# Kernel tuning notes

Measured on AMD Instinct MI355X. Metric: run time of the kernel, lower is better.

Reference implementation:

```python
import jax, jax.numpy as jnp
import numpy as np

N, INC, INN, OUTC, OUTN, MAXD = 8, 64, 20000, 64, 8000, 32


def setup_inputs() -> dict:
    key = jax.random.key(0)
    k0, k1, k2, k3, k4 = jax.random.split(key, 5)
    # adjacency list: outn nodes, degree in [8, 32], padded to MAXD with index 0
    rng = np.random.default_rng(0)
    deg = rng.integers(8, MAXD + 1, size=OUTN)                      # (outn,)
    A_np = rng.integers(0, INN, size=(OUTN, MAXD))                  # (outn, maxD)
    valid = np.arange(MAXD)[None, :] < deg[:, None]
    A_np = np.where(valid, A_np, 0)
    # '_norm' option: mask entries are 1/degree for valid slots, 0 for pad
    mask_np = valid.astype(np.float32) / deg[:, None].astype(np.float32)

    x = jax.random.normal(k0, (N, INC, INN), dtype=jnp.float32)
    # hadamard weight: sqrt(2/inn) * U(-1, 1)
    weight = np.sqrt(2.0 / INN).astype(np.float32) * (
        2.0 * jax.random.uniform(k1, (INC, INN), dtype=jnp.float32) - 1.0)
    # weight_norm Linear(inc, outc): v (outc, inc) direction, g (outc,) magnitude
    ct_v = jax.random.normal(k2, (OUTC, INC), dtype=jnp.float32) * (1.0 / np.sqrt(INC).astype(np.float32))
    ct_g = 0.5 + jax.random.uniform(k3, (OUTC,), dtype=jnp.float32)
    bias = 0.2 * jax.random.normal(k4, (1, OUTC, OUTN), dtype=jnp.float32)
    return {
        'x': x,
        'weight': weight,
        'ct_v': ct_v,
        'ct_g': ct_g,
        'bias': bias,
        'mask': jnp.asarray(mask_np),
        'A': jnp.asarray(A_np, dtype=jnp.int32),
    }


def reference(x, weight, ct_v, ct_g, bias, mask, A):
    # x: (N, inc, inn); weight: (inc, inn)
    xw = x * weight                                   # hadamard
    gathered = xw[:, :, A]                            # (N, inc, outn, maxD) adjacency gather
    pooled = jnp.einsum('bcod,od->bco', gathered, mask)  # degree-normalized masked sum
    # weight_norm: W = g * v / ||v||_row
    W = ct_g[:, None] * ct_v / jnp.linalg.norm(ct_v, axis=1, keepdims=True)  # (outc, inc)
    y = jnp.einsum('bco,kc->bko', pooled, W)          # (N, outc, outn)
    return y + bias
```

## Files before the change

kernel.cpp:

```cpp
#include <hip/hip_runtime.h>
#include <stdint.h>

#define NB   8
#define INC  64
#define INN  20000
#define OUTC 64
#define OUTN 8000
#define MAXD 32

__device__ __forceinline__ uint32_t pack_bf16_2(float a, float b) {
    uint32_t ua = __float_as_uint(a);
    uint32_t ub = __float_as_uint(b);
    uint32_t ra = (ua + 0x7FFFu + ((ua >> 16) & 1u)) >> 16;
    uint32_t rb = (ub + 0x7FFFu + ((ub >> 16) & 1u)) >> 16;
    return (ra & 0xFFFFu) | (rb << 16);
}

__global__ void prep_kernel(const int* __restrict__ A, const float* __restrict__ mask,
                            const float* __restrict__ ct_v, const float* __restrict__ ct_g,
                            uint4* __restrict__ AQ, float2* __restrict__ scale2,
                            float* __restrict__ W_T) {
    if (blockIdx.x == 64) {
        int k = threadIdx.x;
        if (k < OUTC) {
            float s = 0.f;
            for (int c = 0; c < INC; ++c) { float v = ct_v[k * INC + c]; s += v * v; }
            float inv = ct_g[k] / sqrtf(s);
            for (int c = 0; c < INC; ++c) W_T[c * OUTC + k] = ct_v[k * INC + c] * inv;
        }
        return;
    }
    int o = blockIdx.x * 128 + threadIdx.x;
    if (o >= OUTN) return;
    const int4* arow = (const int4*)(A + (size_t)o * MAXD);
#pragma unroll
    for (int j = 0; j < 4; ++j) {
        int4 v0 = arow[2 * j];
        int4 v1 = arow[2 * j + 1];
        uint4 pk;
        pk.x = (uint32_t)v0.x | ((uint32_t)v0.y << 16);
        pk.y = (uint32_t)v0.z | ((uint32_t)v0.w << 16);
        pk.z = (uint32_t)v1.x | ((uint32_t)v1.y << 16);
        pk.w = (uint32_t)v1.z | ((uint32_t)v1.w << 16);
        AQ[(size_t)j * OUTN + o] = pk;
    }
    float invdeg = mask[(size_t)o * MAXD];
    float deg    = rintf(1.0f / invdeg);
    scale2[o] = make_float2(invdeg, 32.0f - deg);
}

__global__ __launch_bounds__(1024, 8)
void gather_kernel(const float* __restrict__ x, const float* __restrict__ w,
                   const uint4* __restrict__ AQ, const float2* __restrict__ scale2,
                   float* __restrict__ pooled) {
    __shared__ __align__(16) uint32_t smem[INN];
    int h = blockIdx.x;
    int g = blockIdx.y;
    int b = blockIdx.z;
    int tid = threadIdx.x;
    int c0 = g * 2;

    const float* xb = x + ((size_t)b * INC + c0) * INN;
    const float* wb = w + (size_t)c0 * INN;
    for (int p = tid; p < INN / 4; p += 1024) {
        int i = p * 4;
        float4 x0 = *(const float4*)(xb + i);
        float4 x1 = *(const float4*)(xb + INN + i);
        float4 w0 = *(const float4*)(wb + i);
        float4 w1 = *(const float4*)(wb + INN + i);
        uint4 pk;
        pk.x = pack_bf16_2(x0.x * w0.x, x1.x * w1.x);
        pk.y = pack_bf16_2(x0.y * w0.y, x1.y * w1.y);
        pk.z = pack_bf16_2(x0.z * w0.z, x1.z * w1.z);
        pk.w = pack_bf16_2(x0.w * w0.w, x1.w * w1.w);
        *(uint4*)&smem[i] = pk;
    }
    __syncthreads();

    uint32_t z = smem[0];
    float z0 = __uint_as_float(z << 16);
    float z1 = __uint_as_float(z & 0xFFFF0000u);

    const char* sbase = (const char*)smem;
    int obase = h * (OUTN / 2);
    int oend  = obase + (OUTN / 2);
#pragma unroll
    for (int it = 0; it < 4; ++it) {
        int o = obase + tid + it * 1024;
        if (o < oend) {
            uint32_t q[16];
#pragma unroll
            for (int j = 0; j < 4; ++j) {
                uint4 v = AQ[(size_t)j * OUTN + o];
                q[j * 4 + 0] = v.x; q[j * 4 + 1] = v.y;
                q[j * 4 + 2] = v.z; q[j * 4 + 3] = v.w;
            }
            float a0 = 0.f, a1 = 0.f;
#pragma unroll
            for (int p = 0; p < 16; ++p) {
                uint32_t u   = q[p];
                int off0 = (int)(u & 0xFFFFu) << 2;
                int off1 = (int)(u >> 16) << 2;
                uint32_t v0 = *(const uint32_t*)(sbase + off0);
                uint32_t v1 = *(const uint32_t*)(sbase + off1);
                a0 += __uint_as_float(v0 << 16);
                a1 += __uint_as_float(v0 & 0xFFFF0000u);
                a0 += __uint_as_float(v1 << 16);
                a1 += __uint_as_float(v1 & 0xFFFF0000u);
            }
            float2 sc = scale2[o];
            a0 = (a0 - sc.y * z0) * sc.x;
            a1 = (a1 - sc.y * z1) * sc.x;
            pooled[((size_t)(b * OUTC + c0 + 0)) * OUTN + o] = a0;
            pooled[((size_t)(b * OUTC + c0 + 1)) * OUTN + o] = a1;
        }
    }
}

__global__ __launch_bounds__(256)
void out_kernel(float* io, const float* __restrict__ W_T,
                const float* __restrict__ bias) {
    __shared__ __align__(16) float sp[INC][128];
    __shared__ __align__(16) float sw[INC][OUTC];
    int obase = blockIdx.x * 128;
    int b     = blockIdx.y;

    const float* pb = io + (size_t)b * INC * OUTN;
    for (int idx = threadIdx.x; idx < INC * 32; idx += 256) {
        int c  = idx >> 5;
        int q  = idx & 31;
        int o4 = obase + q * 4;
        float4 v = (o4 < OUTN) ? *(const float4*)(pb + (size_t)c * OUTN + o4)
                               : make_float4(0.f, 0.f, 0.f, 0.f);
        *(float4*)(&sp[c][q * 4]) = v;
    }
    for (int idx = threadIdx.x; idx < (INC * OUTC) / 4; idx += 256) {
        ((float4*)sw)[idx] = ((const float4*)W_T)[idx];
    }
    __syncthreads();

    int t   = threadIdx.x;
    int kt  = t >> 4;
    int ot0 = (t & 15) * 8;
    int k0  = kt * 4;

    float acc[4][8];
#pragma unroll
    for (int kk = 0; kk < 4; ++kk) {
#pragma unroll
        for (int jh = 0; jh < 2; ++jh) {
            int o4 = obase + ot0 + jh * 4;
            float4 bv = (o4 < OUTN)
                ? *(const float4*)(bias + (size_t)(k0 + kk) * OUTN + o4)
                : make_float4(0.f, 0.f, 0.f, 0.f);
            acc[kk][jh * 4 + 0] = bv.x;
            acc[kk][jh * 4 + 1] = bv.y;
            acc[kk][jh * 4 + 2] = bv.z;
            acc[kk][jh * 4 + 3] = bv.w;
        }
    }

#pragma unroll 4
    for (int c = 0; c < INC; ++c) {
        float4 w4  = *(const float4*)(&sw[c][k0]);
        float4 pa  = *(const float4*)(&sp[c][ot0]);
        float4 pb4 = *(const float4*)(&sp[c][ot0 + 4]);
        float p[8] = {pa.x, pa.y, pa.z, pa.w, pb4.x, pb4.y, pb4.z, pb4.w};
        float wv[4] = {w4.x, w4.y, w4.z, w4.w};
#pragma unroll
        for (int kk = 0; kk < 4; ++kk)
#pragma unroll
            for (int j = 0; j < 8; ++j)
                acc[kk][j] += wv[kk] * p[j];
    }

    int o0 = obase + ot0;
    if (o0 < OUTN) {
#pragma unroll
        for (int kk = 0; kk < 4; ++kk) {
            float4 s0 = make_float4(acc[kk][0], acc[kk][1], acc[kk][2], acc[kk][3]);
            float4 s1 = make_float4(acc[kk][4], acc[kk][5], acc[kk][6], acc[kk][7]);
            float* dst = io + ((size_t)(b * OUTC + k0 + kk)) * OUTN + o0;
            *(float4*)(dst)     = s0;
            *(float4*)(dst + 4) = s1;
        }
    }
}

extern "C" void kernel_launch(void* const* d_in, const int* in_sizes, int n_in,
                              void* d_out, int out_size, void* d_ws, size_t ws_size,
                              hipStream_t stream) {
    const float* x    = (const float*)d_in[0];
    const float* w    = (const float*)d_in[1];
    const float* ct_v = (const float*)d_in[2];
    const float* ct_g = (const float*)d_in[3];
    const float* bias = (const float*)d_in[4];
    const float* mask = (const float*)d_in[5];
    const int*   A    = (const int*)d_in[6];
    float* y = (float*)d_out;

    char* ws = (char*)d_ws;
    uint4*  AQ     = (uint4*)(ws);
    float2* scale2 = (float2*)(ws + 512000);
    float*  W_T    = (float*)(ws + 576000);

    prep_kernel<<<65, 128, 0, stream>>>(A, mask, ct_v, ct_g, AQ, scale2, W_T);
    gather_kernel<<<dim3(2, 32, NB), 1024, 0, stream>>>(x, w, AQ, scale2, y);
    out_kernel<<<dim3(63, NB), 256, 0, stream>>>(y, W_T, bias);
}
```

Baseline: 52.38 us.

## Transpose hadamard product to node-major bf16 and gather rows from global/L2

The prep kernel now computes x*w in bf16 and writes it transposed as (batch, node, channel), so each input node's 64 channels sit in one 128-byte row. The gather kernel assigns one wavefront per output node, with lanes mapping to channels. Neighbour indices are broadcast with readfirstlane, and each neighbour becomes one coalesced row read from global/L2 instead of an LDS gather. Results are transposed through shared memory for coalesced stores. This replaces the per-block 80 KB LDS staging, in which x was reread 2x across halves. The cost is an extra 20 MB workspace round trip and random row accesses that rely on L2/MALL hits.

```diff
diff --git a/kernel.cpp b/kernel.cpp
--- a/kernel.cpp
+++ b/kernel.cpp
@@ -8,111 +8,149 @@
 #define OUTN 8000
 #define MAXD 32
 
-__device__ __forceinline__ uint32_t pack_bf16_2(float a, float b) {
-    uint32_t ua = __float_as_uint(a);
-    uint32_t ub = __float_as_uint(b);
-    uint32_t ra = (ua + 0x7FFFu + ((ua >> 16) & 1u)) >> 16;
-    uint32_t rb = (ub + 0x7FFFu + ((ub >> 16) & 1u)) >> 16;
-    return (ra & 0xFFFFu) | (rb << 16);
-}
-
-__global__ void prep_kernel(const int* __restrict__ A, const float* __restrict__ mask,
-                            const float* __restrict__ ct_v, const float* __restrict__ ct_g,
-                            uint4* __restrict__ AQ, float2* __restrict__ scale2,
-                            float* __restrict__ W_T) {
-    if (blockIdx.x == 64) {
-        int k = threadIdx.x;
-        if (k < OUTC) {
-            float s = 0.f;
-            for (int c = 0; c < INC; ++c) { float v = ct_v[k * INC + c]; s += v * v; }
-            float inv = ct_g[k] / sqrtf(s);
-            for (int c = 0; c < INC; ++c) W_T[c * OUTC + k] = ct_v[k * INC + c] * inv;
-        }
+__global__ __launch_bounds__(256)
+void xt_prep_kernel(const float* __restrict__ x, const float* __restrict__ w,
+                    const int* __restrict__ A, const float* __restrict__ mask,
+                    const float* __restrict__ ct_v, const float* __restrict__ ct_g,
+                    ushort* __restrict__ xT, uint4* __restrict__ AQ,
+                    float2* __restrict__ scale2, float* __restrict__ W_T) {
+    int t = threadIdx.x;
+    if (blockIdx.y == 8) {
+        int flat = blockIdx.x;
+        if (flat == 64) {
+            int k = t;
+            if (k < OUTC) {
+                float s = 0.f;
+                for (int c = 0; c < INC; ++c) { float v = ct_v[k * INC + c]; s += v * v; }
+                float inv = ct_g[k] / sqrtf(s);
+                for (int c = 0; c < INC; ++c) W_T[c * OUTC + k] = ct_v[k * INC + c] * inv;
+            }
+            return;
+        }
+        if (flat > 64 || t >= 128) return;
+        int o = flat * 128 + t;
+        if (o >= OUTN) return;
+        const int4* arow = (const int4*)(A + (size_t)o * MAXD);
+#pragma unroll
+        for (int j = 0; j < 4; ++j) {
+            int4 v0 = arow[2 * j];
+            int4 v1 = arow[2 * j + 1];
+            uint4 pk;
+            pk.x = (uint32_t)(v0.x << 1) | ((uint32_t)(v0.y << 1) << 16);
+            pk.y = (uint32_t)(v0.z << 1) | ((uint32_t)(v0.w << 1) << 16);
+            pk.z = (uint32_t)(v1.x << 1) | ((uint32_t)(v1.y << 1) << 16);
+            pk.w = (uint32_t)(v1.z << 1) | ((uint32_t)(v1.w << 1) << 16);
+            AQ[(size_t)j * OUTN + o] = pk;
+        }
+        float invdeg = mask[(size_t)o * MAXD];
+        float deg    = rintf(1.0f / invdeg);
+        scale2[o] = make_float2(invdeg, 32.0f - deg);
         return;
     }
-    int o = blockIdx.x * 128 + threadIdx.x;
-    if (o >= OUTN) return;
-    const int4* arow = (const int4*)(A + (size_t)o * MAXD);
-#pragma unroll
-    for (int j = 0; j < 4; ++j) {
-        int4 v0 = arow[2 * j];
-        int4 v1 = arow[2 * j + 1];
-        uint4 pk;
-        pk.x = (uint32_t)v0.x | ((uint32_t)v0.y << 16);
-        pk.y = (uint32_t)v0.z | ((uint32_t)v0.w << 16);
-        pk.z = (uint32_t)v1.x | ((uint32_t)v1.y << 16);
-        pk.w = (uint32_t)v1.z | ((uint32_t)v1.w << 16);
-        AQ[(size_t)j * OUTN + o] = pk;
-    }
-    float invdeg = mask[(size_t)o * MAXD];
-    float deg    = rintf(1.0f / invdeg);
-    scale2[o] = make_float2(invdeg, 32.0f - deg);
-}
-
-__global__ __launch_bounds__(1024, 8)
-void gather_kernel(const float* __restrict__ x, const float* __restrict__ w,
-                   const uint4* __restrict__ AQ, const float2* __restrict__ scale2,
-                   float* __restrict__ pooled) {
-    __shared__ __align__(16) uint32_t smem[INN];
-    int h = blockIdx.x;
-    int g = blockIdx.y;
-    int b = blockIdx.z;
-    int tid = threadIdx.x;
-    int c0 = g * 2;
-
-    const float* xb = x + ((size_t)b * INC + c0) * INN;
-    const float* wb = w + (size_t)c0 * INN;
-    for (int p = tid; p < INN / 4; p += 1024) {
-        int i = p * 4;
-        float4 x0 = *(const float4*)(xb + i);
-        float4 x1 = *(const float4*)(xb + INN + i);
-        float4 w0 = *(const float4*)(wb + i);
-        float4 w1 = *(const float4*)(wb + INN + i);
-        uint4 pk;
-        pk.x = pack_bf16_2(x0.x * w0.x, x1.x * w1.x);
-        pk.y = pack_bf16_2(x0.y * w0.y, x1.y * w1.y);
-        pk.z = pack_bf16_2(x0.z * w0.z, x1.z * w1.z);
-        pk.w = pack_bf16_2(x0.w * w0.w, x1.w * w1.w);
-        *(uint4*)&smem[i] = pk;
+
+    __shared__ ushort tile[64][68];
+    int b  = blockIdx.y;
+    int i0 = blockIdx.x * 64;
+    int il = (t & 15) * 4;
+    int cb = t >> 4;
+
+#pragma unroll
+    for (int cl = 0; cl < 4; ++cl) {
+        int c = cb + cl * 16;
+        int i = i0 + il;
+        if (i < INN) {
+            float4 xv = *(const float4*)(x + ((size_t)b * INC + c) * INN + i);
+            float4 wv = *(const float4*)(w + (size_t)c * INN + i);
+            float p0 = xv.x * wv.x, p1 = xv.y * wv.y, p2 = xv.z * wv.z, p3 = xv.w * wv.w;
+            uint32_t u0 = (__float_as_uint(p0) + 0x7FFFu + ((__float_as_uint(p0) >> 16) & 1u)) >> 16;
+            uint32_t u1 = (__float_as_uint(p1) + 0x7FFFu + ((__float_as_uint(p1) >> 16) & 1u)) >> 16;
+            uint32_t u2 = (__float_as_uint(p2) + 0x7FFFu + ((__float_as_uint(p2) >> 16) & 1u)) >> 16;
+            uint32_t u3 = (__float_as_uint(p3) + 0x7FFFu + ((__float_as_uint(p3) >> 16) & 1u)) >> 16;
+            uint2 pk = make_uint2((u0 & 0xFFFFu) | (u1 << 16), (u2 & 0xFFFFu) | (u3 << 16));
+            *(uint2*)(&tile[c][il]) = pk;
+        }
     }
     __syncthreads();
 
-    uint32_t z = smem[0];
-    float z0 = __uint_as_float(z << 16);
-    float z1 = __uint_as_float(z & 0xFFFF0000u);
-
-    const char* sbase = (const char*)smem;
-    int obase = h * (OUTN / 2);
-    int oend  = obase + (OUTN / 2);
-#pragma unroll
-    for (int it = 0; it < 4; ++it) {
-        int o = obase + tid + it * 1024;
-        if (o < oend) {
-            uint32_t q[16];
-#pragma unroll
-            for (int j = 0; j < 4; ++j) {
-                uint4 v = AQ[(size_t)j * OUTN + o];
-                q[j * 4 + 0] = v.x; q[j * 4 + 1] = v.y;
-                q[j * 4 + 2] = v.z; q[j * 4 + 3] = v.w;
+    int i_loc = t >> 2;
+    int h     = t & 3;
+    int i     = i0 + i_loc;
+    if (i < INN) {
+        ushort s[16];
+#pragma unroll
+        for (int j = 0; j < 16; ++j) s[j] = tile[h * 16 + j][i_loc];
+        uint4 a0, a1;
+        a0.x = (uint32_t)s[0]  | ((uint32_t)s[1]  << 16);
+        a0.y = (uint32_t)s[2]  | ((uint32_t)s[3]  << 16);
+        a0.z = (uint32_t)s[4]  | ((uint32_t)s[5]  << 16);
+        a0.w = (uint32_t)s[6]  | ((uint32_t)s[7]  << 16);
+        a1.x = (uint32_t)s[8]  | ((uint32_t)s[9]  << 16);
+        a1.y = (uint32_t)s[10] | ((uint32_t)s[11] << 16);
+        a1.z = (uint32_t)s[12] | ((uint32_t)s[13] << 16);
+        a1.w = (uint32_t)s[14] | ((uint32_t)s[15] << 16);
+        uint32_t* dst = (uint32_t*)(xT + ((size_t)(b * INN + i)) * 64 + h * 16);
+        *(uint4*)(dst)     = a0;
+        *(uint4*)(dst + 4) = a1;
+    }
+}
+
+__global__ __launch_bounds__(256, 8)
+void gather_kernel(const ushort* __restrict__ xT, const uint4* __restrict__ AQ,
+                   const float2* __restrict__ scale2, float* __restrict__ pooled) {
+    __shared__ float trans[128][65];
+    int id    = blockIdx.x;
+    int b     = id & 7;
+    int chunk = id >> 3;
+    int o0    = chunk * 128;
+    int t     = threadIdx.x;
+    int lane  = t & 63;
+    int wid   = t >> 6;
+
+    const char* xTb = (const char*)(xT + (size_t)b * INN * 64);
+    int lane2 = lane * 2;
+    float zv;
+    { ushort u = *(const ushort*)(xTb + lane2); zv = __uint_as_float((uint32_t)u << 16); }
+
+#pragma unroll 2
+    for (int it = 0; it < 32; ++it) {
+        int o = o0 + wid * 32 + it;
+        if (o < OUTN) {
+            uint4 q0 = AQ[o];
+            uint4 q1 = AQ[OUTN + o];
+            uint4 q2 = AQ[2 * OUTN + o];
+            uint4 q3 = AQ[3 * OUTN + o];
+            float acc = 0.f;
+#define DOW(word)                                                               \
+            {                                                                   \
+                uint32_t uu = (uint32_t)__builtin_amdgcn_readfirstlane((int)(word)); \
+                uint32_t lo = (uu & 0xFFFFu) << 6;                              \
+                uint32_t hi = (uu >> 16) << 6;                                  \
+                ushort v0 = *(const ushort*)(xTb + lo + lane2);                 \
+                ushort v1 = *(const ushort*)(xTb + hi + lane2);                 \
+                acc += __uint_as_float((uint32_t)v0 << 16);                     \
+                acc += __uint_as_float((uint32_t)v1 << 16);                     \
             }
-            float a0 = 0.f, a1 = 0.f;
-#pragma unroll
-            for (int p = 0; p < 16; ++p) {
-                uint32_t u   = q[p];
-                int off0 = (int)(u & 0xFFFFu) << 2;
-                int off1 = (int)(u >> 16) << 2;
-                uint32_t v0 = *(const uint32_t*)(sbase + off0);
-                uint32_t v1 = *(const uint32_t*)(sbase + off1);
-                a0 += __uint_as_float(v0 << 16);
-                a1 += __uint_as_float(v0 & 0xFFFF0000u);
-                a0 += __uint_as_float(v1 << 16);
-                a1 += __uint_as_float(v1 & 0xFFFF0000u);
-            }
+            DOW(q0.x) DOW(q0.y) DOW(q0.z) DOW(q0.w)
+            DOW(q1.x) DOW(q1.y) DOW(q1.z) DOW(q1.w)
+            DOW(q2.x) DOW(q2.y) DOW(q2.z) DOW(q2.w)
+            DOW(q3.x) DOW(q3.y) DOW(q3.z) DOW(q3.w)
+#undef DOW
             float2 sc = scale2[o];
-            a0 = (a0 - sc.y * z0) * sc.x;
-            a1 = (a1 - sc.y * z1) * sc.x;
-            pooled[((size_t)(b * OUTC + c0 + 0)) * OUTN + o] = a0;
-            pooled[((size_t)(b * OUTC + c0 + 1)) * OUTN + o] = a1;
+            trans[o - o0][lane] = (acc - sc.y * zv) * sc.x;
+        }
+    }
+    __syncthreads();
+
+    int count = OUTN - o0; if (count > 128) count = 128;
+#pragma unroll
+    for (int rep = 0; rep < 8; ++rep) {
+        int j  = t + rep * 256;
+        int c  = j >> 5;
+        int oq = (j & 31) * 4;
+        if (oq < count) {
+            float4 v = make_float4(trans[oq][c], trans[oq + 1][c],
+                                   trans[oq + 2][c], trans[oq + 3][c]);
+            *(float4*)(pooled + ((size_t)(b * OUTC + c)) * OUTN + o0 + oq) = v;
         }
     }
 }
@@ -200,11 +238,13 @@
     float* y = (float*)d_out;
 
     char* ws = (char*)d_ws;
-    uint4*  AQ     = (uint4*)(ws);
-    float2* scale2 = (float2*)(ws + 512000);
-    float*  W_T    = (float*)(ws + 576000);
-
-    prep_kernel<<<65, 128, 0, stream>>>(A, mask, ct_v, ct_g, AQ, scale2, W_T);
-    gather_kernel<<<dim3(2, 32, NB), 1024, 0, stream>>>(x, w, AQ, scale2, y);
+    ushort* xT     = (ushort*)(ws);
+    uint4*  AQ     = (uint4*)(ws + 20480000);
+    float2* scale2 = (float2*)(ws + 20992000);
+    float*  W_T    = (float*)(ws + 21056000);
+
+    xt_prep_kernel<<<dim3(313, 9), 256, 0, stream>>>(x, w, A, mask, ct_v, ct_g,
+                                                     xT, AQ, scale2, W_T);
+    gather_kernel<<<504, 256, 0, stream>>>(xT, AQ, scale2, y);
     out_kernel<<<dim3(63, NB), 256, 0, stream>>>(y, W_T, bias);
 }
```

After: 70.52 us. +34.6%, slower.
